# Optimization experiments

Measured on AMD Instinct MI355X. Metric: run time of the kernel, lower is better.

Reference implementation:

```python
import jax, jax.numpy as jnp
import numpy as np
import math

HEADS = 8
DIM_HEAD = 64


def setup_inputs() -> dict:
    key = jax.random.key(0)
    k1, k2, k3 = jax.random.split(key, 3)
    b, n, dim = 4, 2048, 512
    inner = HEADS * DIM_HEAD  # 512
    x = jax.random.normal(k1, (b, n, dim), dtype=jnp.float32)
    W_qkv = jax.random.normal(k2, (dim, 4 * inner), dtype=jnp.float32) * (dim ** -0.5)
    W_out = jax.random.normal(k3, (2 * inner, dim), dtype=jnp.float32) * ((2 * inner) ** -0.5)
    b_out = jnp.zeros((dim,), dtype=jnp.float32)
    return {"x": x, "W_qkv": W_qkv, "W_out": W_out, "b_out": b_out}


def reference(x, W_qkv, W_out, b_out):
    b, n, d = x.shape
    h, dh = HEADS, DIM_HEAD
    scale = dh ** -0.5
    qkvt = x @ W_qkv  # [b, n, 4*h*dh]
    q, k, v, t = jnp.split(qkvt, 4, axis=-1)
    # 'b n (h d) -> b h n d'
    def to_heads(z):
        return z.reshape(b, n, h, dh).transpose(0, 2, 1, 3)
    q, k, v, t = map(to_heads, (q, k, v, t))

    # Branch 1: standard softmax attention
    dots = jnp.einsum('bhid,bhjd->bhij', q, k) * scale
    attn1 = jax.nn.softmax(dots, axis=-1)
    out1 = jnp.einsum('bhij,bhjd->bhid', attn1, v)

    # Branch 2: fixed positional-decay attention (shared across b, h; no repeat needed)
    pos = jnp.arange(1, n + 1, dtype=x.dtype)  # linspace(1, n, n)
    tg = jnp.abs(pos[None, :] - pos[:, None])  # |j - i|, [n, n]
    attn2 = jnp.exp(-tg / jnp.asarray(math.e, dtype=x.dtype))
    # NOTE: original divides by sum(-1) WITHOUT keepdim -> broadcasts over columns:
    # attn2[i, j] / sum_k attn2[j, k]
    attn2 = attn2 / attn2.sum(-1)
    out2 = jnp.einsum('ij,bhjd->bhid', attn2, t)

    out = jnp.concatenate([out1, out2], axis=-1)  # [b, h, n, 2*dh]
    out = out.transpose(0, 2, 1, 3).reshape(b, n, 2 * h * dh)  # 'b h n d -> b n (h d)'
    return out @ W_out + b_out
```

## Files before the change

### kernel.cpp

```cpp
#include <hip/hip_runtime.h>
#include <hip/hip_bf16.h>

#define B_ 4
#define N_ 2048
#define D_ 512
#define H_ 8
#define DH_ 64

typedef float float4_ __attribute__((ext_vector_type(4)));
typedef int int2_ __attribute__((ext_vector_type(2)));
typedef int int4_ __attribute__((ext_vector_type(4)));
typedef unsigned short ushort4_ __attribute__((ext_vector_type(4)));
typedef unsigned short ushort8_ __attribute__((ext_vector_type(8)));
typedef __bf16 bf16x8 __attribute__((ext_vector_type(8)));
typedef _Float16 half2_ __attribute__((ext_vector_type(2)));
typedef _Float16 half4_ __attribute__((ext_vector_type(4)));
typedef _Float16 half8_ __attribute__((ext_vector_type(8)));

#if __has_builtin(__builtin_amdgcn_exp2f)
#define EXP2(x) __builtin_amdgcn_exp2f(x)
#else
#define EXP2(x) exp2f(x)
#endif

__device__ __forceinline__ float b2f(unsigned short u) {
  union { unsigned int u; float f; } v; v.u = ((unsigned int)u) << 16; return v.f;
}
__device__ __forceinline__ unsigned short f2b(float f) {
  union { float f; unsigned int u; } v; v.f = f;
  unsigned int r = v.u + 0x7fffu + ((v.u >> 16) & 1u);
  return (unsigned short)(r >> 16);
}
__device__ __forceinline__ half4_ pk4(float a, float b, float c, float d) {
  half2_ lo = __builtin_bit_cast(half2_, __builtin_amdgcn_cvt_pkrtz(a, b));
  half2_ hi = __builtin_bit_cast(half2_, __builtin_amdgcn_cvt_pkrtz(c, d));
  return __builtin_bit_cast(half4_,
      (int2_){__builtin_bit_cast(int, lo), __builtin_bit_cast(int, hi)});
}

#define GLD16(gp, lp)                                                        \
  __builtin_amdgcn_global_load_lds(                                          \
      (const __attribute__((address_space(1))) unsigned int*)(gp),           \
      (__attribute__((address_space(3))) unsigned int*)(lp), 16, 0, 0)

__device__ __forceinline__ bool detect_fp32_local(
    const unsigned short* __restrict__ xhdr, int* cnt_sh) {
  if (threadIdx.x == 0) *cnt_sh = 0;
  __syncthreads();
  unsigned int e = (xhdr[threadIdx.x] >> 7) & 0xFFu;
  if (e >= 134u) atomicAdd(cnt_sh, 1);
  __syncthreads();
  return *cnt_sh > 16;
}

__device__ __forceinline__ void transpose_conv(
    const void* __restrict__ src, unsigned short* __restrict__ dst,
    int R, int C, int bx, int by, bool ofp) {
  __shared__ unsigned short tile[32][33];
  const int c0 = bx * 32, r0 = by * 32;
  const int tx = threadIdx.x & 31, ty = threadIdx.x >> 5;
#pragma unroll
  for (int k = 0; k < 4; ++k) {
    int r = ty + k * 8;
    long idx = (long)(r0 + r) * C + c0 + tx;
    tile[r][tx] = ofp ? f2b(((const float*)src)[idx])
                      : ((const unsigned short*)src)[idx];
  }
  __syncthreads();
#pragma unroll
  for (int k = 0; k < 4; ++k) {
    int c = ty + k * 8;
    dst[(long)(c0 + c) * R + r0 + tx] = tile[tx][c];
  }
}

__global__ __launch_bounds__(256) void prep_all(
    const void* __restrict__ xraw, const void* __restrict__ Wqraw,
    const void* __restrict__ Woraw, unsigned short* __restrict__ xb,
    unsigned short* __restrict__ WqT, unsigned short* __restrict__ WoT,
    unsigned short* __restrict__ Wband) {
  __shared__ int cnt_sh;
  const bool ofp = detect_fp32_local((const unsigned short*)xraw, &cnt_sh);
  const int bid = blockIdx.x;
  if (bid < 4096) {
    int i4 = bid * 256 + threadIdx.x;
    ushort4_ o;
    if (ofp) {
      float4_ v = ((const float4_*)xraw)[i4];
      o[0] = f2b(v[0]); o[1] = f2b(v[1]); o[2] = f2b(v[2]); o[3] = f2b(v[3]);
    } else {
      o = ((const ushort4_*)xraw)[i4];
    }
    *(ushort4_*)(xb + (long)i4 * 4) = o;
  } else if (bid < 5120) {
    const int b2 = bid - 4096;
    transpose_conv(Wqraw, WqT, 512, 2048, b2 % 64, b2 / 64, ofp);
  } else if (bid < 5632) {
    const int b2 = bid - 5120;
    transpose_conv(Woraw, WoT, 1024, 512, b2 % 16, b2 / 16, ofp);
  } else {
    constexpr float INV_E = 0.36787944117144233f;
    constexpr float R1 = 0.69220062755534635f;
    constexpr float INV_1MR = 3.2488706f;
    const int i = bid - 5632;
    const int krel = threadIdx.x;
    const int j = (i >> 6) * 64 - 96 + krel;
    float c = 0.f;
    if (j >= 0 && j < N_) {
      float wgt = __expf(-fabsf((float)(i - j)) * INV_E);
      float rj = __expf(-(float)j * INV_E);
      float rnj = __expf(-(float)(N_ - 1 - j) * INV_E);
      float S = 1.f + R1 * (2.f - rj - rnj) * INV_1MR;
      c = wgt / S;
    }
    _Float16 hv = (_Float16)c;
    Wband[i * 256 + krel] = __builtin_bit_cast(unsigned short, hv);
  }
}

__global__ __launch_bounds__(256) void gemm128(
    const unsigned short* __restrict__ A, const unsigned short* __restrict__ Bt,
    unsigned short* __restrict__ C, int M, int N, int K) {
  __shared__ unsigned short As[128 * 32];
  __shared__ unsigned short Bs[128 * 32];
  const int tid = threadIdx.x;
  const int w = tid >> 6, lane = tid & 63, l16 = lane & 15, quad = lane >> 4;
  const int wm = (w & 1) * 64, wn = (w >> 1) * 64;
  const long tm = (long)blockIdx.x * 128, tn = (long)blockIdx.y * 128;
  const int srow = w * 32 + (lane >> 2);
  const int scol = (lane & 3) * 8;
  float4_ acc[4][4] = {};
  for (int k0 = 0; k0 < K; k0 += 32) {
#pragma unroll
    for (int q = 0; q < 2; ++q) {
      GLD16(&A[(tm + srow + q * 16) * K + k0 + scol], &As[(w * 32 + q * 16) * 32]);
      GLD16(&Bt[(tn + srow + q * 16) * K + k0 + scol], &Bs[(w * 32 + q * 16) * 32]);
    }
    __syncthreads();
    bf16x8 af[4], bf[4];
#pragma unroll
    for (int mb = 0; mb < 4; ++mb)
      af[mb] = __builtin_bit_cast(bf16x8,
          *(const int4_*)&As[(wm + mb * 16 + l16) * 32 + quad * 8]);
#pragma unroll
    for (int nb = 0; nb < 4; ++nb)
      bf[nb] = __builtin_bit_cast(bf16x8,
          *(const int4_*)&Bs[(wn + nb * 16 + l16) * 32 + quad * 8]);
#pragma unroll
    for (int mb = 0; mb < 4; ++mb)
#pragma unroll
      for (int nb = 0; nb < 4; ++nb)
        acc[mb][nb] = __builtin_amdgcn_mfma_f32_16x16x32_bf16(
            af[mb], bf[nb], acc[mb][nb], 0, 0, 0);
    __syncthreads();
  }
#pragma unroll
  for (int nb = 0; nb < 4; ++nb) {
    long col = tn + wn + nb * 16 + l16;
#pragma unroll
    for (int mb = 0; mb < 4; ++mb)
#pragma unroll
      for (int r = 0; r < 4; ++r) {
        long row = tm + wm + mb * 16 + quad * 4 + r;
        C[row * N + col] = f2b(acc[mb][nb][r]);
      }
  }
}

__global__ __launch_bounds__(256) void gemm_n64(
    const unsigned short* __restrict__ A, const unsigned short* __restrict__ Bt,
    void* __restrict__ C, const void* __restrict__ bias_raw,
    int M, int N, int K, const unsigned short* __restrict__ xhdr) {
  __shared__ int cnt_sh;
  const bool ofp = detect_fp32_local(xhdr, &cnt_sh);
  __shared__ unsigned short As[128 * 32];
  __shared__ unsigned short Bs[64 * 32];
  const int tid = threadIdx.x;
  const int w = tid >> 6, lane = tid & 63, l16 = lane & 15, quad = lane >> 4;
  const int wm = (w & 1) * 64, wn = (w >> 1) * 32;
  const long tm = (long)blockIdx.x * 128, tn = (long)blockIdx.y * 64;
  const int srowA = w * 32 + (lane >> 2);
  const int srowB = w * 16 + (lane >> 2);
  const int scol = (lane & 3) * 8;
  float4_ acc[4][2] = {};
  for (int k0 = 0; k0 < K; k0 += 32) {
#pragma unroll
    for (int q = 0; q < 2; ++q)
      GLD16(&A[(tm + srowA + q * 16) * K + k0 + scol], &As[(w * 32 + q * 16) * 32]);
    GLD16(&Bt[(tn + srowB) * K + k0 + scol], &Bs[(w * 16) * 32]);
    __syncthreads();
    bf16x8 af[4], bf[2];
#pragma unroll
    for (int mb = 0; mb < 4; ++mb)
      af[mb] = __builtin_bit_cast(bf16x8,
          *(const int4_*)&As[(wm + mb * 16 + l16) * 32 + quad * 8]);
#pragma unroll
    for (int nb = 0; nb < 2; ++nb)
      bf[nb] = __builtin_bit_cast(bf16x8,
          *(const int4_*)&Bs[(wn + nb * 16 + l16) * 32 + quad * 8]);
#pragma unroll
    for (int mb = 0; mb < 4; ++mb)
#pragma unroll
      for (int nb = 0; nb < 2; ++nb)
        acc[mb][nb] = __builtin_amdgcn_mfma_f32_16x16x32_bf16(
            af[mb], bf[nb], acc[mb][nb], 0, 0, 0);
    __syncthreads();
  }
#pragma unroll
  for (int nb = 0; nb < 2; ++nb) {
    long col = tn + wn + nb * 16 + l16;
    float bv = ofp ? ((const float*)bias_raw)[col]
                   : b2f(((const unsigned short*)bias_raw)[col]);
#pragma unroll
    for (int mb = 0; mb < 4; ++mb)
#pragma unroll
      for (int r = 0; r < 4; ++r) {
        long row = tm + wm + mb * 16 + quad * 4 + r;
        float val = acc[mb][nb][r] + bv;
        if (ofp) ((float*)C)[row * N + col] = val;
        else ((unsigned short*)C)[row * N + col] = f2b(val);
      }
  }
}

#define TTW 2240
__global__ __launch_bounds__(256) void build_vtt(
    const unsigned short* __restrict__ qkvt, unsigned short* __restrict__ Vt,
    unsigned short* __restrict__ Tt) {
  const int z = blockIdx.z;
  if (z == 4) {
    int bid = blockIdx.y * 64 + blockIdx.x;
    int idx4 = (bid * 256 + threadIdx.x) * 4;
    if (idx4 >= 2048 * 192) return;
    int row = idx4 / 192, rem = idx4 % 192;
    int pos = (rem < 96) ? rem : (rem - 96) + 96 + 2048;
    *(ushort4_*)&Tt[(long)row * TTW + pos] = (ushort4_){0, 0, 0, 0};
    return;
  }
  __shared__ unsigned short tile[32][33];
  const int bh = blockIdx.y, b = bh >> 3, h = bh & 7;
  const int j0 = blockIdx.x * 32;
  const bool isv = (z < 2);
  const int d0 = (isv ? z : z - 2) * 32;
  const int srccol = isv ? 1024 : 1536;
  const int tx = threadIdx.x & 31, ty = threadIdx.x >> 5;
#pragma unroll
  for (int k = 0; k < 4; ++k) {
    int j = ty + k * 8;
    tile[j][tx] = qkvt[(long)(b * N_ + j0 + j) * 2048 + srccol + h * 64 + d0 + tx];
  }
  __syncthreads();
#pragma unroll
  for (int k = 0; k < 4; ++k) {
    int dd = ty + k * 8;
    _Float16 hv = (_Float16)b2f(tile[tx][dd]);
    unsigned short us = __builtin_bit_cast(unsigned short, hv);
    if (isv)
      Vt[((long)bh * 64 + d0 + dd) * 2048 + j0 + tx] = us;
    else
      Tt[((long)bh * 64 + d0 + dd) * TTW + 96 + j0 + tx] = us;
  }
}

__global__ __launch_bounds__(256) void branch2_mfma(
    const unsigned short* __restrict__ Wband, const unsigned short* __restrict__ Tt,
    unsigned short* __restrict__ catb) {
  const int qtile = blockIdx.x;
  const int bh = blockIdx.y, b = bh >> 3, h = bh & 7;
  const int tid = threadIdx.x;
  const int w = tid >> 6, lane = tid & 63, l16 = lane & 15, quad = lane >> 4;
  const int i_row = qtile * 64 + w * 16 + l16;
  const unsigned short* ap = Wband + i_row * 256;
  float4_ acc[4] = {};
#pragma unroll
  for (int kh = 0; kh < 8; ++kh) {
    half8_ af = __builtin_bit_cast(half8_, *(const int4_*)&ap[kh * 32 + quad * 8]);
#pragma unroll
    for (int nb = 0; nb < 4; ++nb) {
      half8_ bf = __builtin_bit_cast(half8_,
          *(const int4_*)&Tt[((long)bh * 64 + nb * 16 + l16) * TTW +
                             qtile * 64 + kh * 32 + quad * 8]);
      acc[nb] = __builtin_amdgcn_mfma_f32_16x16x32_f16(af, bf, acc[nb], 0, 0, 0);
    }
  }
#pragma unroll
  for (int nb = 0; nb < 4; ++nb)
#pragma unroll
    for (int r = 0; r < 4; ++r) {
      int row = qtile * 64 + w * 16 + quad * 4 + r;
      catb[(long)(b * N_ + row) * 1024 + h * 128 + 64 + nb * 16 + l16] =
          f2b(acc[nb][r]);
    }
}

__global__ __launch_bounds__(256) void flash_kernel(
    const unsigned short* __restrict__ qkvt, const unsigned short* __restrict__ Vt,
    unsigned short* __restrict__ catb) {
  __shared__ unsigned short Ks[2][64 * 64];
  __shared__ unsigned short Vs[2][64 * 64];
  const int bh = blockIdx.y, b = bh >> 3, h = bh & 7;
  const int i0 = blockIdx.x * 64;
  const int tid = threadIdx.x;
  const int w = tid >> 6, lane = tid & 63, l16 = lane & 15, quad = lane >> 4;
  const int srow8 = lane >> 3, sch = lane & 7;
  const int chK = sch ^ srow8;
  bf16x8 qf[2];
  {
    constexpr float SCL = 0.125f * 1.44269504088896f;
    const long qrow = (long)(b * N_ + i0 + w * 16 + l16) * 2048 + h * 64;
#pragma unroll
    for (int kh = 0; kh < 2; ++kh) {
      ushort8_ raw = __builtin_bit_cast(ushort8_,
          *(const int4_*)&qkvt[qrow + kh * 32 + quad * 8]);
      ushort8_ sc;
#pragma unroll
      for (int e = 0; e < 8; ++e) sc[e] = f2b(b2f(raw[e]) * SCL);
      qf[kh] = __builtin_bit_cast(bf16x8, sc);
    }
  }
  const unsigned short* kp[2];
#pragma unroll
  for (int kh = 0; kh < 2; ++kh)
    kp[kh] = &Ks[0][l16 * 64 + (((kh * 4 + quad) ^ (l16 & 7)) * 8)];
  const unsigned short* vp[4];
#pragma unroll
  for (int c = 0; c < 4; ++c)
    vp[c] = &Vs[0][l16 * 64 + (((c * 2 + (quad >> 1)) ^ (l16 & 7)) * 8) +
                   (quad & 1) * 4];
  const unsigned short* kg[2];
  const unsigned short* vg[2];
#pragma unroll
  for (int g = 0; g < 2; ++g) {
    const int row = w * 16 + g * 8 + srow8;
    kg[g] = qkvt + (long)(b * N_ + row) * 2048 + 512 + h * 64 + chK * 8;
    vg[g] = Vt + ((long)bh * 64 + row) * 2048 + chK * 8;
  }
  float4_ O[4] = {};
  float4_ O5 = {};
  const half4_ ones = {(_Float16)1.f, (_Float16)1.f, (_Float16)1.f, (_Float16)1.f};

  auto stage = [&](int jt_, int buf_) __attribute__((always_inline)) {
    const int j0 = jt_ * 64;
#pragma unroll
    for (int g = 0; g < 2; ++g) {
      GLD16(kg[g] + (long)j0 * 2048,
            (char*)&Ks[0][0] + buf_ * 8192 + (w * 16 + g * 8) * 128);
      GLD16(vg[g] + j0,
            (char*)&Vs[0][0] + buf_ * 8192 + (w * 16 + g * 8) * 128);
    }
  };
  auto phase = [&](int jt_, int buf_) __attribute__((always_inline)) {
    if (jt_ + 1 < 32) stage(jt_ + 1, buf_ ^ 1);
    float4_ s[4] = {};
#pragma unroll
    for (int kh = 0; kh < 2; ++kh)
#pragma unroll
      for (int c = 0; c < 4; ++c) {
        bf16x8 kf = __builtin_bit_cast(bf16x8,
            *(const int4_*)(kp[kh] + buf_ * 4096 + c * 1024));
        s[c] = __builtin_amdgcn_mfma_f32_16x16x32_bf16(kf, qf[kh], s[c], 0, 0, 0);
      }
    half4_ pf[4];
#pragma unroll
    for (int c = 0; c < 4; ++c)
      pf[c] = pk4(EXP2(s[c][0]), EXP2(s[c][1]), EXP2(s[c][2]), EXP2(s[c][3]));
#pragma unroll
    for (int c = 0; c < 4; ++c) {
#pragma unroll
      for (int dblk = 0; dblk < 4; ++dblk) {
        half4_ vfv = *(const half4_*)(vp[c] + buf_ * 4096 + dblk * 1024);
        O[dblk] = __builtin_amdgcn_mfma_f32_16x16x16f16(
            pf[c], vfv, O[dblk], 0, 0, 0);
      }
      O5 = __builtin_amdgcn_mfma_f32_16x16x16f16(pf[c], ones, O5, 0, 0, 0);
    }
    __syncthreads();
  };

  stage(0, 0);
  __syncthreads();
  for (int jt = 0; jt < 32; jt += 2) {
    phase(jt, 0);
    phase(jt + 1, 1);
  }
  float linv[4];
#pragma unroll
  for (int r = 0; r < 4; ++r) linv[r] = 1.f / O5[r];
#pragma unroll
  for (int dblk = 0; dblk < 4; ++dblk)
#pragma unroll
    for (int r = 0; r < 4; ++r) {
      int row = i0 + w * 16 + quad * 4 + r;
      catb[(long)(b * N_ + row) * 1024 + h * 128 + dblk * 16 + l16] =
          f2b(O[dblk][r] * linv[r]);
    }
}

extern "C" void kernel_launch(void* const* d_in, const int* in_sizes, int n_in,
                              void* d_out, int out_size, void* d_ws, size_t ws_size,
                              hipStream_t stream) {
  char* ws = (char*)d_ws;
  unsigned short* qkvt = (unsigned short*)(ws);
  unsigned short* WqT  = (unsigned short*)(ws + (size_t)32 * 1024 * 1024);
  unsigned short* WoT  = (unsigned short*)(ws + (size_t)34 * 1024 * 1024);
  unsigned short* Vt   = (unsigned short*)(ws + (size_t)35 * 1024 * 1024);
  unsigned short* catb = (unsigned short*)(ws + (size_t)43 * 1024 * 1024);
  unsigned short* xb   = (unsigned short*)(ws + (size_t)59 * 1024 * 1024);
  unsigned short* Wband= (unsigned short*)(ws + (size_t)68 * 1024 * 1024);
  unsigned short* Tt   = xb;

  prep_all<<<7680, 256, 0, stream>>>(d_in[0], d_in[1], d_in[2],
                                     xb, WqT, WoT, Wband);
  gemm128<<<dim3(8192 / 128, 2048 / 128), 256, 0, stream>>>(
      xb, WqT, qkvt, 8192, 2048, 512);
  build_vtt<<<dim3(64, 32, 5), 256, 0, stream>>>(qkvt, Vt, Tt);
  branch2_mfma<<<dim3(32, 32), 256, 0, stream>>>(Wband, Tt, catb);
  flash_kernel<<<dim3(2048 / 64, 32), 256, 0, stream>>>(qkvt, Vt, catb);
  gemm_n64<<<dim3(8192 / 128, 512 / 64), 256, 0, stream>>>(
      catb, WoT, d_out, d_in[3], 8192, 512, 1024,
      (const unsigned short*)d_in[0]);
}
```

Baseline: 217.0 us.

## Fuse V transpose and banded branch-2 MFMA into one kernel using shared T tile

Merges build_vtt and branch2_mfma into a single launch. V-transpose blocks stay as before, while branch-2 blocks gather their T window (with zero padding at the edges) straight from qkvt into shared memory. This removes the global Tt round trip, the zero-fill pass and one kernel launch. In exchange the T gather does strided, mostly uncoalesced global reads, each block refetches overlapping T rows, and the ~34KB shared allocation may reduce occupancy for the transpose blocks.

```diff
diff --git a/kernel.cpp b/kernel.cpp
--- a/kernel.cpp
+++ b/kernel.cpp
@@ -223,51 +223,54 @@
   }
 }
 
-#define TTW 2240
-__global__ __launch_bounds__(256) void build_vtt(
+#define TSW 266
+__global__ __launch_bounds__(256) void mid_all(
     const unsigned short* __restrict__ qkvt, unsigned short* __restrict__ Vt,
-    unsigned short* __restrict__ Tt) {
-  const int z = blockIdx.z;
-  if (z == 4) {
-    int bid = blockIdx.y * 64 + blockIdx.x;
-    int idx4 = (bid * 256 + threadIdx.x) * 4;
-    if (idx4 >= 2048 * 192) return;
-    int row = idx4 / 192, rem = idx4 % 192;
-    int pos = (rem < 96) ? rem : (rem - 96) + 96 + 2048;
-    *(ushort4_*)&Tt[(long)row * TTW + pos] = (ushort4_){0, 0, 0, 0};
+    const unsigned short* __restrict__ Wband, unsigned short* __restrict__ catb) {
+  __shared__ unsigned short Ts[64 * TSW];
+  const int bid = blockIdx.x;
+  const int tid = threadIdx.x;
+  if (bid < 4096) {
+    unsigned short (*tile)[33] = (unsigned short (*)[33])Ts;
+    const int j0 = (bid & 63) * 32;
+    const int bh = (bid >> 6) & 31, b = bh >> 3, h = bh & 7;
+    const int d0 = (bid >> 11) * 32;
+    const int tx = tid & 31, ty = tid >> 5;
+#pragma unroll
+    for (int k = 0; k < 4; ++k) {
+      int j = ty + k * 8;
+      tile[j][tx] = qkvt[(long)(b * N_ + j0 + j) * 2048 + 1024 + h * 64 + d0 + tx];
+    }
+    __syncthreads();
+#pragma unroll
+    for (int k = 0; k < 4; ++k) {
+      int dd = ty + k * 8;
+      _Float16 hv = (_Float16)b2f(tile[tx][dd]);
+      Vt[((long)bh * 64 + d0 + dd) * 2048 + j0 + tx] =
+          __builtin_bit_cast(unsigned short, hv);
+    }
     return;
   }
-  __shared__ unsigned short tile[32][33];
-  const int bh = blockIdx.y, b = bh >> 3, h = bh & 7;
-  const int j0 = blockIdx.x * 32;
-  const bool isv = (z < 2);
-  const int d0 = (isv ? z : z - 2) * 32;
-  const int srccol = isv ? 1024 : 1536;
-  const int tx = threadIdx.x & 31, ty = threadIdx.x >> 5;
-#pragma unroll
-  for (int k = 0; k < 4; ++k) {
-    int j = ty + k * 8;
-    tile[j][tx] = qkvt[(long)(b * N_ + j0 + j) * 2048 + srccol + h * 64 + d0 + tx];
+  const int b2 = bid - 4096;
+  const int qtile = b2 & 31;
+  const int bh = b2 >> 5, b = bh >> 3, h = bh & 7;
+  const int jlo = qtile * 64 - 96;
+  {
+    const int d = tid & 63;
+    const int kkb = tid >> 6;
+#pragma unroll
+    for (int it = 0; it < 64; ++it) {
+      const int kk = it * 4 + kkb;
+      const int j = jlo + kk;
+      unsigned short us = 0;
+      if (j >= 0 && j < N_) {
+        _Float16 hv = (_Float16)b2f(qkvt[(long)(b * N_ + j) * 2048 + 1536 + h * 64 + d]);
+        us = __builtin_bit_cast(unsigned short, hv);
+      }
+      Ts[d * TSW + kk] = us;
+    }
   }
   __syncthreads();
-#pragma unroll
-  for (int k = 0; k < 4; ++k) {
-    int dd = ty + k * 8;
-    _Float16 hv = (_Float16)b2f(tile[tx][dd]);
-    unsigned short us = __builtin_bit_cast(unsigned short, hv);
-    if (isv)
-      Vt[((long)bh * 64 + d0 + dd) * 2048 + j0 + tx] = us;
-    else
-      Tt[((long)bh * 64 + d0 + dd) * TTW + 96 + j0 + tx] = us;
-  }
-}
-
-__global__ __launch_bounds__(256) void branch2_mfma(
-    const unsigned short* __restrict__ Wband, const unsigned short* __restrict__ Tt,
-    unsigned short* __restrict__ catb) {
-  const int qtile = blockIdx.x;
-  const int bh = blockIdx.y, b = bh >> 3, h = bh & 7;
-  const int tid = threadIdx.x;
   const int w = tid >> 6, lane = tid & 63, l16 = lane & 15, quad = lane >> 4;
   const int i_row = qtile * 64 + w * 16 + l16;
   const unsigned short* ap = Wband + i_row * 256;
@@ -278,8 +281,7 @@
 #pragma unroll
     for (int nb = 0; nb < 4; ++nb) {
       half8_ bf = __builtin_bit_cast(half8_,
-          *(const int4_*)&Tt[((long)bh * 64 + nb * 16 + l16) * TTW +
-                             qtile * 64 + kh * 32 + quad * 8]);
+          *(const int4_*)&Ts[(nb * 16 + l16) * TSW + kh * 32 + quad * 8]);
       acc[nb] = __builtin_amdgcn_mfma_f32_16x16x32_f16(af, bf, acc[nb], 0, 0, 0);
     }
   }
@@ -407,14 +409,12 @@
   unsigned short* catb = (unsigned short*)(ws + (size_t)43 * 1024 * 1024);
   unsigned short* xb   = (unsigned short*)(ws + (size_t)59 * 1024 * 1024);
   unsigned short* Wband= (unsigned short*)(ws + (size_t)68 * 1024 * 1024);
-  unsigned short* Tt   = xb;
 
   prep_all<<<7680, 256, 0, stream>>>(d_in[0], d_in[1], d_in[2],
                                      xb, WqT, WoT, Wband);
   gemm128<<<dim3(8192 / 128, 2048 / 128), 256, 0, stream>>>(
       xb, WqT, qkvt, 8192, 2048, 512);
-  build_vtt<<<dim3(64, 32, 5), 256, 0, stream>>>(qkvt, Vt, Tt);
-  branch2_mfma<<<dim3(32, 32), 256, 0, stream>>>(Wband, Tt, catb);
+  mid_all<<<5120, 256, 0, stream>>>(qkvt, Vt, Wband, catb);
   flash_kernel<<<dim3(2048 / 64, 32), 256, 0, stream>>>(qkvt, Vt, catb);
   gemm_n64<<<dim3(8192 / 128, 512 / 64), 256, 0, stream>>>(
       catb, WoT, d_out, d_in[3], 8192, 512, 1024,
```

Result: no change. 213.4 us (-1.6%).
